# Kernel tuning notes

Measured on AMD Instinct MI355X. Metric: run time of the kernel, lower is better.

The kernel has to match this reference:

```python
import jax, jax.numpy as jnp
import numpy as np
from jax import lax

PALETTE = 256


def setup_inputs() -> dict:
    key = jax.random.key(0)
    k1, k2, k3, k4 = jax.random.split(key, 4)
    x = jax.random.normal(k1, (16, 64, 256, 256), dtype=jnp.float32)
    lookup_table = jax.random.normal(k2, (PALETTE,), dtype=jnp.float32) * 0.05
    weight_idx = jax.random.randint(k3, (64, 64, 3, 3), 0, PALETTE, dtype=jnp.int32)
    bias = jax.random.normal(k4, (64,), dtype=jnp.float32) * 0.01
    return {"x": x, "lookup_table": lookup_table, "weight_idx": weight_idx, "bias": bias}


def reference(x, lookup_table, weight_idx, bias):
    # Dequantize: palette gather produces full OIHW weight tensor.
    full_w = lookup_table[weight_idx]  # [O, I, kH, kW] float32
    # conv2d with stride=1, padding=0 (hardcoded in module), dilation=1, groups=1
    out = lax.conv_general_dilated(
        x, full_w,
        window_strides=(1, 1),
        padding='VALID',
        rhs_dilation=(1, 1),
        dimension_numbers=('NCHW', 'OIHW', 'NCHW'),
        feature_group_count=1,
    )
    return out + bias[None, :, None, None]
```

## Files before the change

kernel.cpp:

```cpp
#include <hip/hip_runtime.h>
#include <hip/hip_bf16.h>


typedef __bf16 bf16x8 __attribute__((ext_vector_type(8)));
typedef float f32x4 __attribute__((ext_vector_type(4)));

union Frag {
    uint4 q;
    bf16x8 v;
};

__global__ __launch_bounds__(256) void dequant_B(
        const float* __restrict__ lut, const int* __restrict__ widx,
        uint4* __restrict__ Bws) {
    int s = blockIdx.x * 256 + threadIdx.x;
    int l = s & 63;
    int nt = (s >> 6) & 3;
    int kc = s >> 8;
    if (kc >= 18) return;
    int r = kc >> 1;
    int kh = r / 3, kw = r - kh * 3;
    int o = nt * 16 + (l & 15);
    int c0 = (kc & 1) * 32 + (l >> 4) * 8;
    Frag f;
#pragma unroll
    for (int j = 0; j < 8; ++j) {
        int c = c0 + j;
        int idx = widx[((o * 64 + c) * 3 + kh) * 3 + kw];
        f.v[j] = (__bf16)lut[idx];
    }
    Bws[s] = f.q;
}

#define LDS_PIX 396

__global__ __launch_bounds__(256, 3) void conv_mfma(
        const float* __restrict__ x, const float* __restrict__ bias,
        const uint4* __restrict__ Bws, float* __restrict__ out) {
    __shared__ uint4 ldsA[8 * LDS_PIX];

    int bx = blockIdx.x;
    int ow0 = (bx & 3) * 64;
    int oh0 = ((bx >> 2) & 63) * 4;
    int n = bx >> 8;
    int t = threadIdx.x;

    {
        const float* xn = x + (size_t)n * (64 * 256 * 256);
        int col = t & 63;
        int cbb = t >> 6;
#pragma unroll
        for (int cp = 0; cp < 2; ++cp) {
            int cblk = cbb + cp * 4;
#pragma unroll
            for (int rr = 0; rr < 6; ++rr) {
                int y = oh0 + rr; if (y > 255) y = 255;
                const float* src = xn + cblk * 8 * 65536 + y * 256 + ow0 + col;
                Frag f;
#pragma unroll
                for (int j = 0; j < 8; ++j)
                    f.v[j] = (__bf16)src[j * 65536];
                ldsA[cblk * LDS_PIX + rr * 66 + col] = f.q;
            }
        }
        if (t < 96) {
            int cblk = t & 7;
            int rc = t >> 3;
            int rr = rc >> 1;
            int col2 = 64 + (rc & 1);
            int y = oh0 + rr; if (y > 255) y = 255;
            int xc = ow0 + col2; if (xc > 255) xc = 255;
            const float* src = xn + cblk * 8 * 65536 + y * 256 + xc;
            Frag f;
#pragma unroll
            for (int j = 0; j < 8; ++j)
                f.v[j] = (__bf16)src[j * 65536];
            ldsA[cblk * LDS_PIX + rr * 66 + col2] = f.q;
        }
    }
    __syncthreads();

    int w = t >> 6;
    int l = t & 63;
    int l15 = l & 15, l4 = l >> 4;

    f32x4 acc[4][4] = {};

    for (int kc = 0; kc < 18; ++kc) {
        int r = kc >> 1;
        int kh = r / 3, kw = r - kh * 3;
        int cblk = (kc & 1) * 4 + l4;
        int pix = (w + kh) * 66 + l15 + kw;

        Frag b[4];
#pragma unroll
        for (int nt = 0; nt < 4; ++nt)
            b[nt].q = Bws[(kc * 4 + nt) * 64 + l];

        Frag a[4];
#pragma unroll
        for (int mt = 0; mt < 4; ++mt)
            a[mt].q = ldsA[cblk * LDS_PIX + pix + mt * 16];

#pragma unroll
        for (int mt = 0; mt < 4; ++mt)
#pragma unroll
            for (int nt = 0; nt < 4; ++nt)
                acc[mt][nt] = __builtin_amdgcn_mfma_f32_16x16x32_bf16(
                    a[mt].v, b[nt].v, acc[mt][nt], 0, 0, 0);
    }

    int oh = oh0 + w;
    if (oh < 254) {
#pragma unroll
        for (int nt = 0; nt < 4; ++nt) {
            int o = nt * 16 + l15;
            float bv = bias[o];
            float* obase = out + (((size_t)n * 64 + o) * 254 + oh) * 254 + ow0;
#pragma unroll
            for (int mt = 0; mt < 4; ++mt) {
#pragma unroll
                for (int rg = 0; rg < 4; ++rg) {
                    int owl = mt * 16 + l4 * 4 + rg;
                    if (ow0 + owl < 254)
                        obase[owl] = acc[mt][nt][rg] + bv;
                }
            }
        }
    }
}

extern "C" void kernel_launch(void* const* d_in, const int* in_sizes, int n_in,
                              void* d_out, int out_size, void* d_ws, size_t ws_size,
                              hipStream_t stream) {
    const float* x    = (const float*)d_in[0];
    const float* lut  = (const float*)d_in[1];
    const int*   widx = (const int*)d_in[2];
    const float* bias = (const float*)d_in[3];
    float* out = (float*)d_out;
    uint4* Bws = (uint4*)d_ws;

    dequant_B<<<18, 256, 0, stream>>>(lut, widx, Bws);
    conv_mfma<<<4096, 256, 0, stream>>>(x, bias, (const uint4*)Bws, out);
}
```

Measured before the change: 519.2 us.

## Pipeline input staging with MFMA compute across two row tiles per block

Each block now handles two 4-row output tiles, and processes the channel halves in separate regions so that global loads for the next half-tile are issued while MFMAs run on the current one, overlapping staging with compute. Block indices are swizzled across XCDs, the grid is halved, and the epilogue stores use paired 2-wide float writes. The cost is higher register pressure from the prefetch buffers and more barriers, which could lower occupancy.

```diff
diff --git a/kernel.cpp b/kernel.cpp
--- a/kernel.cpp
+++ b/kernel.cpp
@@ -1,14 +1,19 @@
 #include <hip/hip_runtime.h>
-#include <hip/hip_bf16.h>
 
 
 typedef __bf16 bf16x8 __attribute__((ext_vector_type(8)));
 typedef float f32x4 __attribute__((ext_vector_type(4)));
+typedef float f32x2 __attribute__((ext_vector_type(2)));
 
 union Frag {
     uint4 q;
     bf16x8 v;
 };
+
+#define LGKM_BARRIER() do { \
+    asm volatile("s_waitcnt lgkmcnt(0)" ::: "memory"); \
+    __builtin_amdgcn_s_barrier(); \
+    asm volatile("" ::: "memory"); } while (0)
 
 __global__ __launch_bounds__(256) void dequant_B(
         const float* __restrict__ lut, const int* __restrict__ widx,
@@ -40,94 +45,159 @@
     __shared__ uint4 ldsA[8 * LDS_PIX];
 
     int bx = blockIdx.x;
-    int ow0 = (bx & 3) * 64;
-    int oh0 = ((bx >> 2) & 63) * 4;
-    int n = bx >> 8;
+    int swz = (bx & 7) * 256 + (bx >> 3);
+    int ow0 = (swz & 3) * 64;
+    int ohp = (swz >> 2) & 31;
+    int n   = swz >> 7;
+    int oh0a = ohp * 8;
+    int oh0b = oh0a + 4;
+
     int t = threadIdx.x;
-
-    {
-        const float* xn = x + (size_t)n * (64 * 256 * 256);
-        int col = t & 63;
-        int cbb = t >> 6;
-#pragma unroll
-        for (int cp = 0; cp < 2; ++cp) {
-            int cblk = cbb + cp * 4;
-#pragma unroll
-            for (int rr = 0; rr < 6; ++rr) {
-                int y = oh0 + rr; if (y > 255) y = 255;
-                const float* src = xn + cblk * 8 * 65536 + y * 256 + ow0 + col;
+    int w = t >> 6, l = t & 63;
+    int l15 = l & 15, l4 = l >> 4;
+
+    const float* xn = x + (size_t)n * (64 * 256 * 256);
+
+    int tl_cb  = t & 3;
+    int tl_rc  = t >> 2;
+    int tl_rr  = tl_rc >> 1;
+    int tl_col = 64 + (tl_rc & 1);
+    int tl_xc  = ow0 + tl_col; if (tl_xc > 255) tl_xc = 255;
+
+    f32x4 acc[4][4];
+
+    auto stage_plain = [&](int half, int oh0s) {
+        const float* sb = xn + (half * 4 + w) * 524288 + ow0 + l;
+#pragma unroll
+        for (int j = 0; j < 6; ++j) {
+            int y = oh0s + j; if (y > 255) y = 255;
+            const float* src = sb + y * 256;
+            Frag f;
+#pragma unroll
+            for (int jj = 0; jj < 8; ++jj)
+                f.v[jj] = (__bf16)src[jj * 65536];
+            ldsA[(half * 4 + w) * LDS_PIX + j * 66 + l] = f.q;
+        }
+        if (t < 48) {
+            int y = oh0s + tl_rr; if (y > 255) y = 255;
+            const float* src = xn + (half * 4 + tl_cb) * 524288 + y * 256 + tl_xc;
+            Frag f;
+#pragma unroll
+            for (int jj = 0; jj < 8; ++jj)
+                f.v[jj] = (__bf16)src[jj * 65536];
+            ldsA[(half * 4 + tl_cb) * LDS_PIX + tl_rr * 66 + tl_col] = f.q;
+        }
+    };
+
+    auto region = [&](int PAR, bool STAGE, int shalf, int oh0s) {
+        float pre[4][8];
+        const float* sb = xn + (shalf * 4 + w) * 524288 + ow0 + l;
+#pragma unroll
+        for (int i = 0; i < 9; ++i) {
+            if (STAGE && i < 7) {
+                if (i < 6) {
+                    int y = oh0s + i; if (y > 255) y = 255;
+                    const float* src = sb + y * 256;
+#pragma unroll
+                    for (int jj = 0; jj < 8; ++jj)
+                        pre[i & 3][jj] = src[jj * 65536];
+                } else if (t < 48) {
+                    int y = oh0s + tl_rr; if (y > 255) y = 255;
+                    const float* src = xn + (shalf * 4 + tl_cb) * 524288 + y * 256 + tl_xc;
+#pragma unroll
+                    for (int jj = 0; jj < 8; ++jj)
+                        pre[6 & 3][jj] = src[jj * 65536];
+                }
+            }
+            {
+                int kh = i / 3, kw = i - kh * 3;
+                int cblk = PAR * 4 + l4;
+                int pix = (w + kh) * 66 + l15 + kw;
+                int kc = 2 * i + PAR;
+                Frag b[4];
+#pragma unroll
+                for (int nt = 0; nt < 4; ++nt)
+                    b[nt].q = Bws[(kc * 4 + nt) * 64 + l];
+                Frag a[4];
+#pragma unroll
+                for (int mt = 0; mt < 4; ++mt)
+                    a[mt].q = ldsA[cblk * LDS_PIX + pix + mt * 16];
+#pragma unroll
+                for (int mt = 0; mt < 4; ++mt)
+#pragma unroll
+                    for (int nt = 0; nt < 4; ++nt)
+                        acc[mt][nt] = __builtin_amdgcn_mfma_f32_16x16x32_bf16(
+                            a[mt].v, b[nt].v, acc[mt][nt], 0, 0, 0);
+            }
+            if (STAGE && i >= 3) {
+                int jd = i - 3;
                 Frag f;
 #pragma unroll
-                for (int j = 0; j < 8; ++j)
-                    f.v[j] = (__bf16)src[j * 65536];
-                ldsA[cblk * LDS_PIX + rr * 66 + col] = f.q;
-            }
-        }
-        if (t < 96) {
-            int cblk = t & 7;
-            int rc = t >> 3;
-            int rr = rc >> 1;
-            int col2 = 64 + (rc & 1);
-            int y = oh0 + rr; if (y > 255) y = 255;
-            int xc = ow0 + col2; if (xc > 255) xc = 255;
-            const float* src = xn + cblk * 8 * 65536 + y * 256 + xc;
+                for (int jj = 0; jj < 8; ++jj)
+                    f.v[jj] = (__bf16)pre[jd & 3][jj];
+                ldsA[(shalf * 4 + w) * LDS_PIX + jd * 66 + l] = f.q;
+            }
+        }
+        if (STAGE && t < 48) {
             Frag f;
 #pragma unroll
-            for (int j = 0; j < 8; ++j)
-                f.v[j] = (__bf16)src[j * 65536];
-            ldsA[cblk * LDS_PIX + rr * 66 + col2] = f.q;
-        }
-    }
-    __syncthreads();
-
-    int w = t >> 6;
-    int l = t & 63;
-    int l15 = l & 15, l4 = l >> 4;
-
-    f32x4 acc[4][4] = {};
-
-    for (int kc = 0; kc < 18; ++kc) {
-        int r = kc >> 1;
-        int kh = r / 3, kw = r - kh * 3;
-        int cblk = (kc & 1) * 4 + l4;
-        int pix = (w + kh) * 66 + l15 + kw;
-
-        Frag b[4];
+            for (int jj = 0; jj < 8; ++jj)
+                f.v[jj] = (__bf16)pre[6 & 3][jj];
+            ldsA[(shalf * 4 + tl_cb) * LDS_PIX + tl_rr * 66 + tl_col] = f.q;
+        }
+    };
+
+    auto epilogue = [&](int oh0t) {
+        int oh = oh0t + w;
+        if (oh < 254) {
+#pragma unroll
+            for (int nt = 0; nt < 4; ++nt) {
+                int o = nt * 16 + l15;
+                float bv = bias[o];
+                float* ob = out + (((size_t)n * 64 + o) * 254 + oh) * 254 + ow0;
+#pragma unroll
+                for (int mt = 0; mt < 4; ++mt) {
+                    int owl = mt * 16 + l4 * 4;
+                    f32x4 v;
+#pragma unroll
+                    for (int rg = 0; rg < 4; ++rg)
+                        v[rg] = acc[mt][nt][rg] + bv;
+                    if (ow0 + owl + 3 < 254) {
+                        *(f32x2*)(ob + owl)     = f32x2{v[0], v[1]};
+                        *(f32x2*)(ob + owl + 2) = f32x2{v[2], v[3]};
+                    } else {
+#pragma unroll
+                        for (int rg = 0; rg < 4; ++rg)
+                            if (ow0 + owl + rg < 254)
+                                ob[owl + rg] = v[rg];
+                    }
+                }
+            }
+        }
+    };
+
+#pragma unroll
+    for (int mt = 0; mt < 4; ++mt)
 #pragma unroll
         for (int nt = 0; nt < 4; ++nt)
-            b[nt].q = Bws[(kc * 4 + nt) * 64 + l];
-
-        Frag a[4];
-#pragma unroll
-        for (int mt = 0; mt < 4; ++mt)
-            a[mt].q = ldsA[cblk * LDS_PIX + pix + mt * 16];
-
-#pragma unroll
-        for (int mt = 0; mt < 4; ++mt)
-#pragma unroll
-            for (int nt = 0; nt < 4; ++nt)
-                acc[mt][nt] = __builtin_amdgcn_mfma_f32_16x16x32_bf16(
-                    a[mt].v, b[nt].v, acc[mt][nt], 0, 0, 0);
-    }
-
-    int oh = oh0 + w;
-    if (oh < 254) {
-#pragma unroll
-        for (int nt = 0; nt < 4; ++nt) {
-            int o = nt * 16 + l15;
-            float bv = bias[o];
-            float* obase = out + (((size_t)n * 64 + o) * 254 + oh) * 254 + ow0;
-#pragma unroll
-            for (int mt = 0; mt < 4; ++mt) {
-#pragma unroll
-                for (int rg = 0; rg < 4; ++rg) {
-                    int owl = mt * 16 + l4 * 4 + rg;
-                    if (ow0 + owl < 254)
-                        obase[owl] = acc[mt][nt][rg] + bv;
-                }
-            }
-        }
-    }
+            acc[mt][nt] = f32x4{0.f, 0.f, 0.f, 0.f};
+
+    stage_plain(0, oh0a);
+    LGKM_BARRIER();
+    region(0, true, 1, oh0a);
+    LGKM_BARRIER();
+    region(1, true, 0, oh0b);
+    epilogue(oh0a);
+#pragma unroll
+    for (int mt = 0; mt < 4; ++mt)
+#pragma unroll
+        for (int nt = 0; nt < 4; ++nt)
+            acc[mt][nt] = f32x4{0.f, 0.f, 0.f, 0.f};
+    LGKM_BARRIER();
+    region(0, true, 1, oh0b);
+    LGKM_BARRIER();
+    region(1, false, 0, 0);
+    epilogue(oh0b);
 }
 
 extern "C" void kernel_launch(void* const* d_in, const int* in_sizes, int n_in,
@@ -141,5 +211,5 @@
     uint4* Bws = (uint4*)d_ws;
 
     dequant_B<<<18, 256, 0, stream>>>(lut, widx, Bws);
-    conv_mfma<<<4096, 256, 0, stream>>>(x, bias, (const uint4*)Bws, out);
+    conv_mfma<<<2048, 256, 0, stream>>>(x, bias, (const uint4*)Bws, out);
 }
```

After: 662.0 us. 1.28x slower.

## Stage input channels in two halves to halve LDS and double occupancy

Applied to the files above, without the earlier changes.

The input tile is now loaded into LDS in two passes of 32 channels each instead of all 64 at once, and the 9-tap MFMA loop runs after each pass. This halves the LDS footprint per block and raises the launch bound to allow 6 blocks per CU, aiming to hide global-load latency through more resident waves. In exchange it adds an extra barrier round and serializes loading with compute inside each block, and the higher launch bound tightens the register budget, which could cause spills.

```diff
diff --git a/kernel.cpp b/kernel.cpp
--- a/kernel.cpp
+++ b/kernel.cpp
@@ -1,5 +1,4 @@
 #include <hip/hip_runtime.h>
-#include <hip/hip_bf16.h>
 
 
 typedef __bf16 bf16x8 __attribute__((ext_vector_type(8)));
@@ -34,10 +33,10 @@
 
 #define LDS_PIX 396
 
-__global__ __launch_bounds__(256, 3) void conv_mfma(
+__global__ __launch_bounds__(256, 6) void conv_mfma(
         const float* __restrict__ x, const float* __restrict__ bias,
         const uint4* __restrict__ Bws, float* __restrict__ out) {
-    __shared__ uint4 ldsA[8 * LDS_PIX];
+    __shared__ uint4 ldsA[4 * LDS_PIX];
 
     int bx = blockIdx.x;
     int ow0 = (bx & 3) * 64;
@@ -45,69 +44,71 @@
     int n = bx >> 8;
     int t = threadIdx.x;
 
-    {
-        const float* xn = x + (size_t)n * (64 * 256 * 256);
-        int col = t & 63;
-        int cbb = t >> 6;
-#pragma unroll
-        for (int cp = 0; cp < 2; ++cp) {
-            int cblk = cbb + cp * 4;
-#pragma unroll
-            for (int rr = 0; rr < 6; ++rr) {
-                int y = oh0 + rr; if (y > 255) y = 255;
-                const float* src = xn + cblk * 8 * 65536 + y * 256 + ow0 + col;
-                Frag f;
-#pragma unroll
-                for (int j = 0; j < 8; ++j)
-                    f.v[j] = (__bf16)src[j * 65536];
-                ldsA[cblk * LDS_PIX + rr * 66 + col] = f.q;
-            }
-        }
-        if (t < 96) {
-            int cblk = t & 7;
-            int rc = t >> 3;
-            int rr = rc >> 1;
-            int col2 = 64 + (rc & 1);
-            int y = oh0 + rr; if (y > 255) y = 255;
-            int xc = ow0 + col2; if (xc > 255) xc = 255;
-            const float* src = xn + cblk * 8 * 65536 + y * 256 + xc;
-            Frag f;
-#pragma unroll
-            for (int j = 0; j < 8; ++j)
-                f.v[j] = (__bf16)src[j * 65536];
-            ldsA[cblk * LDS_PIX + rr * 66 + col2] = f.q;
-        }
-    }
-    __syncthreads();
+    const float* xn = x + (size_t)n * (64 * 256 * 256);
 
     int w = t >> 6;
     int l = t & 63;
     int l15 = l & 15, l4 = l >> 4;
 
+    int st_col = t & 63;
+    int st_cb  = t >> 6;
+    int tl_cb  = t & 3;
+    int tl_rc  = t >> 2;
+    int tl_rr  = tl_rc >> 1;
+    int tl_col = 64 + (tl_rc & 1);
+    int tl_xc  = ow0 + tl_col; if (tl_xc > 255) tl_xc = 255;
+
     f32x4 acc[4][4] = {};
 
-    for (int kc = 0; kc < 18; ++kc) {
-        int r = kc >> 1;
-        int kh = r / 3, kw = r - kh * 3;
-        int cblk = (kc & 1) * 4 + l4;
-        int pix = (w + kh) * 66 + l15 + kw;
-
-        Frag b[4];
+    for (int h = 0; h < 2; ++h) {
+        {
+            const float* sb = xn + (h * 4 + st_cb) * (8 * 65536) + ow0 + st_col;
 #pragma unroll
-        for (int nt = 0; nt < 4; ++nt)
-            b[nt].q = Bws[(kc * 4 + nt) * 64 + l];
-
-        Frag a[4];
+            for (int rr = 0; rr < 6; ++rr) {
+                int y = oh0 + rr; if (y > 255) y = 255;
+                const float* src = sb + y * 256;
+                Frag f;
 #pragma unroll
-        for (int mt = 0; mt < 4; ++mt)
-            a[mt].q = ldsA[cblk * LDS_PIX + pix + mt * 16];
+                for (int j = 0; j < 8; ++j)
+                    f.v[j] = (__bf16)src[j * 65536];
+                ldsA[st_cb * LDS_PIX + rr * 66 + st_col] = f.q;
+            }
+            if (t < 48) {
+                int y = oh0 + tl_rr; if (y > 255) y = 255;
+                const float* src = xn + (h * 4 + tl_cb) * (8 * 65536) + y * 256 + tl_xc;
+                Frag f;
+#pragma unroll
+                for (int j = 0; j < 8; ++j)
+                    f.v[j] = (__bf16)src[j * 65536];
+                ldsA[tl_cb * LDS_PIX + tl_rr * 66 + tl_col] = f.q;
+            }
+        }
+        __syncthreads();
 
 #pragma unroll
-        for (int mt = 0; mt < 4; ++mt)
+        for (int i = 0; i < 9; ++i) {
+            int kh = i / 3, kw = i - kh * 3;
+            int kc = 2 * i + h;
+            int pix = (w + kh) * 66 + l15 + kw;
+
+            Frag b[4];
 #pragma unroll
             for (int nt = 0; nt < 4; ++nt)
-                acc[mt][nt] = __builtin_amdgcn_mfma_f32_16x16x32_bf16(
-                    a[mt].v, b[nt].v, acc[mt][nt], 0, 0, 0);
+                b[nt].q = Bws[(kc * 4 + nt) * 64 + l];
+
+            Frag a[4];
+#pragma unroll
+            for (int mt = 0; mt < 4; ++mt)
+                a[mt].q = ldsA[l4 * LDS_PIX + pix + mt * 16];
+
+#pragma unroll
+            for (int mt = 0; mt < 4; ++mt)
+#pragma unroll
+                for (int nt = 0; nt < 4; ++nt)
+                    acc[mt][nt] = __builtin_amdgcn_mfma_f32_16x16x32_bf16(
+                        a[mt].v, b[nt].v, acc[mt][nt], 0, 0, 0);
+        }
+        if (h == 0) __syncthreads();
     }
 
     int oh = oh0 + w;
```

After: 1.153 ms. 122% more time.
